# Optimization experiments

Measured on AMD Instinct MI355X. Metric: run time of the kernel, lower is better.

The kernel has to match this reference:

```python
import jax, jax.numpy as jnp
import numpy as np

B, S, D, H = 4, 2048, 1024, 16
HD = D // H

def _linear_params(key, fan_in, fan_out):
    kw, kb = jax.random.split(key)
    bound = 1.0 / np.sqrt(fan_in)
    W = jax.random.uniform(kw, (fan_in, fan_out), minval=-bound, maxval=bound, dtype=jnp.float32)
    b = jax.random.uniform(kb, (fan_out,), minval=-bound, maxval=bound, dtype=jnp.float32)
    return W, b

def setup_inputs() -> dict:
    key = jax.random.key(0)
    ks = jax.random.split(key, 7)
    query = jax.random.normal(ks[0], (B, S, D), dtype=jnp.float32)
    key_t = jax.random.normal(ks[1], (B, S, D), dtype=jnp.float32)
    value = jax.random.normal(ks[2], (B, S, D), dtype=jnp.float32)
    Wq, bq = _linear_params(ks[3], D, D)
    Wk, bk = _linear_params(ks[4], D, D)
    Wv, bv = _linear_params(ks[5], D, D)
    Wo, bo = _linear_params(ks[6], D, D)
    return {"query": query, "key": key_t, "value": value,
            "Wq": Wq, "bq": bq, "Wk": Wk, "bk": bk,
            "Wv": Wv, "bv": bv, "Wo": Wo, "bo": bo}

def reference(query, key, value, Wq, bq, Wk, bk, Wv, bv, Wo, bo):
    b, s, _ = query.shape
    scale = HD ** -0.5
    # project and split heads -> [b, h, s, hd]
    Q = (query @ Wq + bq).reshape(b, s, H, HD).transpose(0, 2, 1, 3)
    K = (key @ Wk + bk).reshape(b, s, H, HD).transpose(0, 2, 1, 3)
    V = (value @ Wv + bv).reshape(b, s, H, HD).transpose(0, 2, 1, 3)
    scores = jnp.einsum('bhqd,bhkd->bhqk', Q, K) * scale  # [b,h,s,s]
    attn = jax.nn.softmax(scores, axis=-1)
    out = jnp.einsum('bhqk,bhkd->bhqd', attn, V)
    out = out.transpose(0, 2, 1, 3).reshape(b, s, D)
    return out @ Wo + bo
```

## Files before the change

kernel.cpp:

```cpp
#include <hip/hip_runtime.h>

typedef unsigned short u16;
typedef __attribute__((ext_vector_type(8))) short short8;
typedef __attribute__((ext_vector_type(4))) float f32x4;
typedef __attribute__((ext_vector_type(4))) unsigned int u32x4;

union V8 { u32x4 u; short8 s; };

__device__ __forceinline__ u16 f2bf(float f) {
  union { float f; unsigned u; } v; v.f = f;
  unsigned r = v.u + 0x7fffu + ((v.u >> 16) & 1u);
  return (u16)(r >> 16);
}

__device__ __forceinline__ unsigned cvt_pk_bf16(float lo, float hi) {
  unsigned r;
  asm("v_cvt_pk_bf16_f32 %0, %1, %2" : "=v"(r) : "v"(lo), "v"(hi));
  return r;
}

__device__ __forceinline__ void gload_lds16(const void* g, void* l) {
  __builtin_amdgcn_global_load_lds((const __attribute__((address_space(1))) unsigned int*)g,
                                   (__attribute__((address_space(3))) unsigned int*)l, 16, 0, 0);
}

__device__ __forceinline__ f32x4 mfma16(short8 a, short8 b, f32x4 c) {
  return __builtin_amdgcn_mfma_f32_16x16x32_bf16(a, b, c, 0, 0, 0);
}

__global__ __launch_bounds__(256) void cvt3_kernel(const float* __restrict__ q,
                                                   const float* __restrict__ k,
                                                   const float* __restrict__ v,
                                                   u16* __restrict__ oq,
                                                   u16* __restrict__ ok,
                                                   u16* __restrict__ ov) {
  const int bid = blockIdx.x;
  const float* in = (bid < 4096) ? q : (bid < 8192 ? k : v);
  u16* out = (bid < 4096) ? oq : (bid < 8192 ? ok : ov);
  const size_t i = ((size_t)(bid & 4095) * 256 + threadIdx.x) * 8;
  const float4* p = (const float4*)(in + i);
  float4 a = p[0], b = p[1];
  u32x4 w;
  w[0] = cvt_pk_bf16(a.x, a.y); w[1] = cvt_pk_bf16(a.z, a.w);
  w[2] = cvt_pk_bf16(b.x, b.y); w[3] = cvt_pk_bf16(b.z, b.w);
  *(u32x4*)(out + i) = w;
}

__global__ __launch_bounds__(256) void wtrans4_kernel(const float* __restrict__ Wq, const float* __restrict__ Wk,
                                                      const float* __restrict__ Wv, const float* __restrict__ Wo,
                                                      u16* __restrict__ WtQ, u16* __restrict__ WtK,
                                                      u16* __restrict__ WtV, u16* __restrict__ WtO) {
  const int bid = blockIdx.x;
  const int wsel = bid >> 9;
  const float* W = (wsel == 0) ? Wq : (wsel == 1) ? Wk : (wsel == 2) ? Wv : Wo;
  u16* Wt = (wsel == 0) ? WtQ : (wsel == 1) ? WtK : (wsel == 2) ? WtV : WtO;
  const int tid = (bid & 511) * 256 + threadIdx.x;
  const int n = tid & 1023;
  const int kb = (tid >> 10) << 3;
  u32x4 w;
#pragma unroll
  for (int j = 0; j < 4; j++)
    w[j] = cvt_pk_bf16(W[(size_t)(kb + 2 * j) * 1024 + n], W[(size_t)(kb + 2 * j + 1) * 1024 + n]);
  *(u32x4*)(Wt + (size_t)n * 1024 + kb) = w;
}

__global__ __launch_bounds__(256) void gemm_qkv_kernel(const u16* __restrict__ A,
                                                       const u16* __restrict__ Wt,
                                                       const float* __restrict__ bq,
                                                       const float* __restrict__ bk,
                                                       const float* __restrict__ bv,
                                                       u16* __restrict__ Outs,
                                                       float qscale) {
  constexpr int K = 1024, N = 1024;
  __shared__ u16 Ash[2][4096];
  __shared__ u16 Bsh[2][4096];
  const int t = threadIdx.x;
  const int l = t & 63;
  const int w = t >> 6;
  const int wm = w >> 1, wn = w & 1;
  const int bid0 = blockIdx.x;
  const int swz = (bid0 & 7) * 192 + (bid0 >> 3);
  const int bm = swz >> 3, bn = swz & 7;
  const int m0 = bm * 128, n0 = bn * 128;
  const int sec = m0 >> 13;
  const u16* Bt = Wt + ((size_t)sec << 20);
  const float* bias = (sec == 0) ? bq : (sec == 1) ? bk : bv;
  const float outscale = (sec == 0) ? qscale : 1.0f;

  f32x4 acc[4][4];
#pragma unroll
  for (int i = 0; i < 4; i++)
#pragma unroll
    for (int j = 0; j < 4; j++) acc[i][j] = (f32x4){0.f, 0.f, 0.f, 0.f};

  const int line0 = t >> 3, c8 = t & 7;
  const int lc0 = c8 ^ (line0 & 7);
  const int row0 = 2 * line0 + (lc0 >> 2);
  const int kc0 = (lc0 & 3) << 3;
  const int line1 = line0 + 32;
  const int lc1 = c8 ^ (line1 & 7);
  const int row1 = 2 * line1 + (lc1 >> 2);
  const int kc1 = (lc1 & 3) << 3;

  const u16* Ab = A + (size_t)m0 * K;
  const u16* Bb = Bt + (size_t)n0 * K;

  int aoff[4], boff[4];
#pragma unroll
  for (int mt = 0; mt < 4; mt++) {
    int R = wm * 64 + mt * 16 + (l & 15);
    int cc = (((R & 1) << 2) + (l >> 4)) ^ ((R >> 1) & 7);
    aoff[mt] = (R >> 1) * 64 + cc * 8;
  }
#pragma unroll
  for (int nt = 0; nt < 4; nt++) {
    int R = wn * 64 + nt * 16 + (l & 15);
    int cc = (((R & 1) << 2) + (l >> 4)) ^ ((R >> 1) & 7);
    boff[nt] = (R >> 1) * 64 + cc * 8;
  }

  auto stage = [&](int buf, int k0) {
    u16* AW = &Ash[buf][w * 512];
    u16* BW = &Bsh[buf][w * 512];
    gload_lds16(Ab + (size_t)row0 * K + k0 + kc0, AW);
    gload_lds16(Ab + (size_t)row1 * K + k0 + kc1, AW + 2048);
    gload_lds16(Bb + (size_t)row0 * K + k0 + kc0, BW);
    gload_lds16(Bb + (size_t)row1 * K + k0 + kc1, BW + 2048);
  };

  stage(0, 0);
  __syncthreads();
  int cur = 0;
  for (int k0 = 0; k0 < K; k0 += 32) {
    if (k0 + 32 < K) stage(cur ^ 1, k0 + 32);
    short8 af[4], bfr[4];
#pragma unroll
    for (int mt = 0; mt < 4; mt++) af[mt] = *(const short8*)&Ash[cur][aoff[mt]];
#pragma unroll
    for (int nt = 0; nt < 4; nt++) bfr[nt] = *(const short8*)&Bsh[cur][boff[nt]];
#pragma unroll
    for (int mt = 0; mt < 4; mt++)
#pragma unroll
      for (int nt = 0; nt < 4; nt++)
        acc[mt][nt] = mfma16(af[mt], bfr[nt], acc[mt][nt]);
    __syncthreads();
    cur ^= 1;
  }

#pragma unroll
  for (int nt = 0; nt < 4; nt++) {
    const int n = n0 + wn * 64 + nt * 16 + (l & 15);
    const float bv2 = bias[n];
    if (sec < 2) {
      u16* C = Outs + ((size_t)sec << 23);
#pragma unroll
      for (int mt = 0; mt < 4; mt++) {
        const int m = (m0 & 8191) + wm * 64 + mt * 16 + ((l >> 4) << 2);
#pragma unroll
        for (int r = 0; r < 4; r++)
          C[(size_t)(m + r) * N + n] = f2bf((acc[mt][nt][r] + bv2) * outscale);
      }
    } else {
      const int mloc = m0 & 8191;
      const int b2 = mloc >> 11;
      const int h2 = n >> 6, d = n & 63;
      u16* C = Outs + ((size_t)2 << 23);
#pragma unroll
      for (int mt = 0; mt < 4; mt++) {
        const int s0 = (mloc & 2047) + wm * 64 + mt * 16 + ((l >> 4) << 2);
        const int u = s0 & 63;
        const int pos = ((((u >> 2) & 3) + ((u >> 5) & 1) * 4) << 3) + ((u >> 4) & 1) * 4;
        const int sp = (s0 & ~63) + pos;
        ushort4 pk;
        pk.x = f2bf(acc[mt][nt][0] + bv2);
        pk.y = f2bf(acc[mt][nt][1] + bv2);
        pk.z = f2bf(acc[mt][nt][2] + bv2);
        pk.w = f2bf(acc[mt][nt][3] + bv2);
        *(ushort4*)(C + (((size_t)((b2 * 16 + h2) * 64 + d)) << 11) + sp) = pk;
      }
    }
  }
}

__global__ __launch_bounds__(256) void gemm_out_kernel(const u16* __restrict__ A,
                                                       const u16* __restrict__ Bt,
                                                       const float* __restrict__ bias,
                                                       float* __restrict__ Cout) {
  constexpr int K = 1024, N = 1024;
  __shared__ u16 Ash[2][4096];
  __shared__ u16 Bsh[2][4096];
  const int t = threadIdx.x;
  const int l = t & 63;
  const int w = t >> 6;
  const int wm = w >> 1, wn = w & 1;
  const int bid0 = blockIdx.x;
  const int swz = (bid0 & 7) * 64 + (bid0 >> 3);
  const int bm = swz >> 3, bn = swz & 7;
  const int m0 = bm * 128, n0 = bn * 128;

  f32x4 acc[4][4];
#pragma unroll
  for (int i = 0; i < 4; i++)
#pragma unroll
    for (int j = 0; j < 4; j++) acc[i][j] = (f32x4){0.f, 0.f, 0.f, 0.f};

  const int line0 = t >> 3, c8 = t & 7;
  const int lc0 = c8 ^ (line0 & 7);
  const int row0 = 2 * line0 + (lc0 >> 2);
  const int kc0 = (lc0 & 3) << 3;
  const int line1 = line0 + 32;
  const int lc1 = c8 ^ (line1 & 7);
  const int row1 = 2 * line1 + (lc1 >> 2);
  const int kc1 = (lc1 & 3) << 3;

  const u16* Ab = A + (size_t)m0 * K;
  const u16* Bb = Bt + (size_t)n0 * K;

  int aoff[4], boff[4];
#pragma unroll
  for (int mt = 0; mt < 4; mt++) {
    int R = wm * 64 + mt * 16 + (l & 15);
    int cc = (((R & 1) << 2) + (l >> 4)) ^ ((R >> 1) & 7);
    aoff[mt] = (R >> 1) * 64 + cc * 8;
  }
#pragma unroll
  for (int nt = 0; nt < 4; nt++) {
    int R = wn * 64 + nt * 16 + (l & 15);
    int cc = (((R & 1) << 2) + (l >> 4)) ^ ((R >> 1) & 7);
    boff[nt] = (R >> 1) * 64 + cc * 8;
  }

  auto stage = [&](int buf, int k0) {
    u16* AW = &Ash[buf][w * 512];
    u16* BW = &Bsh[buf][w * 512];
    gload_lds16(Ab + (size_t)row0 * K + k0 + kc0, AW);
    gload_lds16(Ab + (size_t)row1 * K + k0 + kc1, AW + 2048);
    gload_lds16(Bb + (size_t)row0 * K + k0 + kc0, BW);
    gload_lds16(Bb + (size_t)row1 * K + k0 + kc1, BW + 2048);
  };

  stage(0, 0);
  __syncthreads();
  int cur = 0;
  for (int k0 = 0; k0 < K; k0 += 32) {
    if (k0 + 32 < K) stage(cur ^ 1, k0 + 32);
    short8 af[4], bfr[4];
#pragma unroll
    for (int mt = 0; mt < 4; mt++) af[mt] = *(const short8*)&Ash[cur][aoff[mt]];
#pragma unroll
    for (int nt = 0; nt < 4; nt++) bfr[nt] = *(const short8*)&Bsh[cur][boff[nt]];
#pragma unroll
    for (int mt = 0; mt < 4; mt++)
#pragma unroll
      for (int nt = 0; nt < 4; nt++)
        acc[mt][nt] = mfma16(af[mt], bfr[nt], acc[mt][nt]);
    __syncthreads();
    cur ^= 1;
  }

#pragma unroll
  for (int nt = 0; nt < 4; nt++) {
    const int n = n0 + wn * 64 + nt * 16 + (l & 15);
    const float bv2 = bias[n];
#pragma unroll
    for (int mt = 0; mt < 4; mt++) {
      const int m = m0 + wm * 64 + mt * 16 + ((l >> 4) << 2);
#pragma unroll
      for (int r = 0; r < 4; r++)
        Cout[(size_t)(m + r) * N + n] = acc[mt][nt][r] + bv2;
    }
  }
}

__device__ __forceinline__ void softmax_lite(const f32x4 (&s)[4], float& lsum,
                                             short8& pa0, short8& pa1) {
  float p[4][4];
#pragma unroll
  for (int c = 0; c < 4; c++)
#pragma unroll
    for (int r = 0; r < 4; r++) p[c][r] = __builtin_amdgcn_exp2f(s[c][r]);
  lsum += (((p[0][0] + p[0][1]) + (p[0][2] + p[0][3])) + ((p[1][0] + p[1][1]) + (p[1][2] + p[1][3])))
        + (((p[2][0] + p[2][1]) + (p[2][2] + p[2][3])) + ((p[3][0] + p[3][1]) + (p[3][2] + p[3][3])));
  V8 u0, u1;
  u0.u[0] = cvt_pk_bf16(p[0][0], p[0][1]); u0.u[1] = cvt_pk_bf16(p[0][2], p[0][3]);
  u0.u[2] = cvt_pk_bf16(p[1][0], p[1][1]); u0.u[3] = cvt_pk_bf16(p[1][2], p[1][3]);
  u1.u[0] = cvt_pk_bf16(p[2][0], p[2][1]); u1.u[1] = cvt_pk_bf16(p[2][2], p[2][3]);
  u1.u[2] = cvt_pk_bf16(p[3][0], p[3][1]); u1.u[3] = cvt_pk_bf16(p[3][2], p[3][3]);
  pa0 = u0.s; pa1 = u1.s;
}

__global__ __launch_bounds__(256) void attn_kernel(const u16* __restrict__ Qb,
                                                   const u16* __restrict__ Kb,
                                                   const u16* __restrict__ Vtb,
                                                   u16* __restrict__ AO) {
  __shared__ u16 Ksh[2][4096];
  __shared__ u16 Vsh[2][4096];
  const int t = threadIdx.x, l = t & 63, w = t >> 6;
  const int g = l >> 4, ql = l & 15;
  const int bid0 = blockIdx.x;
  const int bid = (bid0 & 7) * 128 + (bid0 >> 3);
  const int qt = bid & 15;
  const int bh = bid >> 4;
  const int h = bh & 15, b = bh >> 4;
  const int q0 = qt * 128 + w * 32;

  const u16* Qrow = Qb + ((size_t)b * 2048 + q0 + ql) * 1024 + h * 64 + g * 8;
  const short8 qA0 = *(const short8*)(Qrow);
  const short8 qA1 = *(const short8*)(Qrow + 32);
  const short8 qB0 = *(const short8*)(Qrow + 16 * 1024);
  const short8 qB1 = *(const short8*)(Qrow + 16 * 1024 + 32);

  float lA = 0.f, lB = 0.f;
  f32x4 oA[4], oB[4];
#pragma unroll
  for (int i = 0; i < 4; i++) { oA[i] = (f32x4){0.f, 0.f, 0.f, 0.f}; oB[i] = oA[i]; }

  const int srow0 = t >> 3, sc = t & 7;
  const int slc0 = sc ^ (srow0 & 7);
  const int srow1 = srow0 + 32, slc1 = sc ^ (srow1 & 7);
  const u16* Kbase = Kb + ((size_t)b * 2048) * 1024 + h * 64;
  const u16* Vbase = Vtb + ((size_t)(b * 16 + h) * 64) * 2048;

  auto stage = [&](int buf, int kk0) {
    u16* KW = &Ksh[buf][w * 512];
    u16* VW = &Vsh[buf][w * 512];
    gload_lds16(Kbase + (size_t)(kk0 + srow0) * 1024 + slc0 * 8, KW);
    gload_lds16(Kbase + (size_t)(kk0 + srow1) * 1024 + slc1 * 8, KW + 2048);
    gload_lds16(Vbase + (size_t)srow0 * 2048 + kk0 + slc0 * 8, VW);
    gload_lds16(Vbase + (size_t)srow1 * 2048 + kk0 + slc1 * 8, VW + 2048);
  };

  int voff0[4], voff1[4];
#pragma unroll
  for (int dt = 0; dt < 4; dt++) {
    const int d = dt * 16 + ql;
    voff0[dt] = d * 64 + ((g ^ (d & 7)) << 3);
    voff1[dt] = d * 64 + (((g + 4) ^ (d & 7)) << 3);
  }

  stage(0, 0);
  __syncthreads();
  int cur = 0;

  for (int kk0 = 0; kk0 < 2048; kk0 += 64) {
    if (kk0 + 64 < 2048) stage(cur ^ 1, kk0 + 64);
    const u16* KC = Ksh[cur];
    const u16* VC = Vsh[cur];

    f32x4 sA[4], sB[4];
    __builtin_amdgcn_s_setprio(1);
#pragma unroll
    for (int c = 0; c < 4; c++) {
      const int R = c * 16 + ql;
      const int x = R & 7;
      const short8 kf0 = *(const short8*)&KC[R * 64 + ((g ^ x) << 3)];
      const short8 kf1 = *(const short8*)&KC[R * 64 + (((g + 4) ^ x) << 3)];
      f32x4 z = (f32x4){0.f, 0.f, 0.f, 0.f};
      z = mfma16(kf0, qA0, z);
      sA[c] = mfma16(kf1, qA1, z);
      z = (f32x4){0.f, 0.f, 0.f, 0.f};
      z = mfma16(kf0, qB0, z);
      sB[c] = mfma16(kf1, qB1, z);
    }
    __builtin_amdgcn_s_setprio(0);

    short8 paA0, paA1, paB0, paB1;
    softmax_lite(sA, lA, paA0, paA1);
    softmax_lite(sB, lB, paB0, paB1);

    __builtin_amdgcn_s_setprio(1);
#pragma unroll
    for (int dt = 0; dt < 4; dt++) {
      const short8 vf0 = *(const short8*)&VC[voff0[dt]];
      const short8 vf1 = *(const short8*)&VC[voff1[dt]];
      oA[dt] = mfma16(paA0, vf0, oA[dt]);
      oA[dt] = mfma16(paA1, vf1, oA[dt]);
      oB[dt] = mfma16(paB0, vf0, oB[dt]);
      oB[dt] = mfma16(paB1, vf1, oB[dt]);
    }
    __builtin_amdgcn_s_setprio(0);
    __syncthreads();
    cur ^= 1;
  }

  lA += __shfl_xor(lA, 16); lA += __shfl_xor(lA, 32);
  lB += __shfl_xor(lB, 16); lB += __shfl_xor(lB, 32);
  const float iA = __builtin_amdgcn_rcpf(lA);
  const float iB = __builtin_amdgcn_rcpf(lB);
  const int sb = g << 2;
  const float iA0 = __shfl(iA, sb), iA1 = __shfl(iA, sb + 1);
  const float iA2 = __shfl(iA, sb + 2), iA3 = __shfl(iA, sb + 3);
  const float iB0 = __shfl(iB, sb), iB1 = __shfl(iB, sb + 1);
  const float iB2 = __shfl(iB, sb + 2), iB3 = __shfl(iB, sb + 3);
  u16* Arow = AO + ((size_t)b * 2048 + q0) * 1024 + h * 64;
#pragma unroll
  for (int dt = 0; dt < 4; dt++) {
    const int col = dt * 16 + ql;
    Arow[(size_t)(4 * g + 0) * 1024 + col] = f2bf(oA[dt][0] * iA0);
    Arow[(size_t)(4 * g + 1) * 1024 + col] = f2bf(oA[dt][1] * iA1);
    Arow[(size_t)(4 * g + 2) * 1024 + col] = f2bf(oA[dt][2] * iA2);
    Arow[(size_t)(4 * g + 3) * 1024 + col] = f2bf(oA[dt][3] * iA3);
    Arow[(size_t)(16 + 4 * g + 0) * 1024 + col] = f2bf(oB[dt][0] * iB0);
    Arow[(size_t)(16 + 4 * g + 1) * 1024 + col] = f2bf(oB[dt][1] * iB1);
    Arow[(size_t)(16 + 4 * g + 2) * 1024 + col] = f2bf(oB[dt][2] * iB2);
    Arow[(size_t)(16 + 4 * g + 3) * 1024 + col] = f2bf(oB[dt][3] * iB3);
  }
}

extern "C" void kernel_launch(void* const* d_in, const int* in_sizes, int n_in,
                              void* d_out, int out_size, void* d_ws, size_t ws_size,
                              hipStream_t stream) {
  (void)in_sizes; (void)n_in; (void)out_size; (void)ws_size;
  const float* query = (const float*)d_in[0];
  const float* key   = (const float*)d_in[1];
  const float* value = (const float*)d_in[2];
  const float* Wq = (const float*)d_in[3];  const float* bq = (const float*)d_in[4];
  const float* Wk = (const float*)d_in[5];  const float* bk = (const float*)d_in[6];
  const float* Wv = (const float*)d_in[7];  const float* bv = (const float*)d_in[8];
  const float* Wo = (const float*)d_in[9];  const float* bo = (const float*)d_in[10];
  float* out = (float*)d_out;

  const size_t SZX = (size_t)8192 * 1024;
  const size_t SZW = (size_t)1024 * 1024;
  u16* qin = (u16*)d_ws;
  u16* kin = qin + SZX;
  u16* vin = kin + SZX;
  u16* Qb  = vin + SZX;
  u16* Kbf = Qb + SZX;
  u16* Vtb = Kbf + SZX;
  u16* WtQ = Vtb + SZX;
  u16* WtK = WtQ + SZW;
  u16* WtV = WtK + SZW;
  u16* WtO = WtV + SZW;
  u16* AO  = qin;

  const float QSCALE = 0.125f * 1.44269504088896f;

  cvt3_kernel<<<12288, 256, 0, stream>>>(query, key, value, qin, kin, vin);
  wtrans4_kernel<<<2048, 256, 0, stream>>>(Wq, Wk, Wv, Wo, WtQ, WtK, WtV, WtO);

  gemm_qkv_kernel<<<1536, 256, 0, stream>>>(qin, WtQ, bq, bk, bv, Qb, QSCALE);

  attn_kernel<<<1024, 256, 0, stream>>>(Qb, Kbf, Vtb, AO);

  gemm_out_kernel<<<512, 256, 0, stream>>>(AO, WtO, bo, out);
}
```

Measured before the change: 337.8 us.

## Merge projection GEMMs into 256x128-tile kernel with triple-buffered interleaved staging

Replaces the two 128x128 GEMM kernels with one templated kernel that uses 256x128 tiles, a three-stage LDS ring buffer, and split staging interleaved between two MFMA half-steps with s_setprio and explicit vmcnt waits. Larger tiles raise operand reuse per LDS load, and the deeper pipeline aims to hide global-load latency. The cost is more accumulator registers and LDS per block. The output GEMM now launches only 256 blocks, which may underfill the 256 CUs.

```diff
diff --git a/kernel.cpp b/kernel.cpp
--- a/kernel.cpp
+++ b/kernel.cpp
@@ -64,210 +64,169 @@
   *(u32x4*)(Wt + (size_t)n * 1024 + kb) = w;
 }
 
-__global__ __launch_bounds__(256) void gemm_qkv_kernel(const u16* __restrict__ A,
-                                                       const u16* __restrict__ Wt,
-                                                       const float* __restrict__ bq,
-                                                       const float* __restrict__ bk,
-                                                       const float* __restrict__ bv,
-                                                       u16* __restrict__ Outs,
-                                                       float qscale) {
-  constexpr int K = 1024, N = 1024;
-  __shared__ u16 Ash[2][4096];
-  __shared__ u16 Bsh[2][4096];
-  const int t = threadIdx.x;
-  const int l = t & 63;
-  const int w = t >> 6;
+template <int IS_QKV>
+__global__ __launch_bounds__(256, 2) void gemm256_kernel(const u16* __restrict__ A,
+                                                         const u16* __restrict__ Wt,
+                                                         const float* __restrict__ bQ,
+                                                         const float* __restrict__ bK,
+                                                         const float* __restrict__ bV,
+                                                         void* __restrict__ Outs,
+                                                         float qscale) {
+  constexpr int K = 1024;
+  constexpr int NBM = IS_QKV ? 96 : 32;
+  constexpr int NT = 32;
+  __shared__ u16 Ash[3][8192];
+  __shared__ u16 Bsh[3][4096];
+  const int t = threadIdx.x, l = t & 63, w = t >> 6;
   const int wm = w >> 1, wn = w & 1;
-  const int bid0 = blockIdx.x;
-  const int swz = (bid0 & 7) * 192 + (bid0 >> 3);
-  const int bm = swz >> 3, bn = swz & 7;
-  const int m0 = bm * 128, n0 = bn * 128;
-  const int sec = m0 >> 13;
+  const int g = l >> 4, ql = l & 15;
+  const int bid = blockIdx.x;
+  const int s = (bid & 7) * NBM + (bid >> 3);
+  const int bm = s >> 3, bn = s & 7;
+  const int m0 = bm * 256, n0 = bn * 128;
+
+  const int sec = IS_QKV ? (bm >> 5) : 0;
   const u16* Bt = Wt + ((size_t)sec << 20);
-  const float* bias = (sec == 0) ? bq : (sec == 1) ? bk : bv;
-  const float outscale = (sec == 0) ? qscale : 1.0f;
-
-  f32x4 acc[4][4];
-#pragma unroll
-  for (int i = 0; i < 4; i++)
-#pragma unroll
-    for (int j = 0; j < 4; j++) acc[i][j] = (f32x4){0.f, 0.f, 0.f, 0.f};
-
-  const int line0 = t >> 3, c8 = t & 7;
-  const int lc0 = c8 ^ (line0 & 7);
-  const int row0 = 2 * line0 + (lc0 >> 2);
-  const int kc0 = (lc0 & 3) << 3;
-  const int line1 = line0 + 32;
-  const int lc1 = c8 ^ (line1 & 7);
-  const int row1 = 2 * line1 + (lc1 >> 2);
-  const int kc1 = (lc1 & 3) << 3;
-
   const u16* Ab = A + (size_t)m0 * K;
   const u16* Bb = Bt + (size_t)n0 * K;
 
-  int aoff[4], boff[4];
-#pragma unroll
-  for (int mt = 0; mt < 4; mt++) {
-    int R = wm * 64 + mt * 16 + (l & 15);
-    int cc = (((R & 1) << 2) + (l >> 4)) ^ ((R >> 1) & 7);
+  f32x4 acc[8][4];
+#pragma unroll
+  for (int i = 0; i < 8; i++)
+#pragma unroll
+    for (int j = 0; j < 4; j++) acc[i][j] = (f32x4){0.f, 0.f, 0.f, 0.f};
+
+  const int slc = (t & 7) ^ ((t >> 3) & 7);
+  const int srow = 2 * (t >> 3) + (slc >> 2);
+  const int skc = (slc & 3) << 3;
+
+  int aoff[8], boff[4];
+#pragma unroll
+  for (int mt = 0; mt < 8; mt++) {
+    const int R = wm * 128 + mt * 16 + ql;
+    const int cc = (((R & 1) << 2) + g) ^ ((R >> 1) & 7);
     aoff[mt] = (R >> 1) * 64 + cc * 8;
   }
 #pragma unroll
   for (int nt = 0; nt < 4; nt++) {
-    int R = wn * 64 + nt * 16 + (l & 15);
-    int cc = (((R & 1) << 2) + (l >> 4)) ^ ((R >> 1) & 7);
+    const int R = wn * 64 + nt * 16 + ql;
+    const int cc = (((R & 1) << 2) + g) ^ ((R >> 1) & 7);
     boff[nt] = (R >> 1) * 64 + cc * 8;
   }
 
-  auto stage = [&](int buf, int k0) {
-    u16* AW = &Ash[buf][w * 512];
-    u16* BW = &Bsh[buf][w * 512];
-    gload_lds16(Ab + (size_t)row0 * K + k0 + kc0, AW);
-    gload_lds16(Ab + (size_t)row1 * K + k0 + kc1, AW + 2048);
-    gload_lds16(Bb + (size_t)row0 * K + k0 + kc0, BW);
-    gload_lds16(Bb + (size_t)row1 * K + k0 + kc1, BW + 2048);
+  auto stA = [&](int buf, int k0s, int j) {
+    gload_lds16(Ab + (size_t)(srow + 64 * j) * K + k0s + skc, &Ash[buf][j * 2048 + w * 512]);
   };
-
-  stage(0, 0);
-  __syncthreads();
+  auto stB = [&](int buf, int k0s, int j) {
+    gload_lds16(Bb + (size_t)(srow + 64 * j) * K + k0s + skc, &Bsh[buf][j * 2048 + w * 512]);
+  };
+
+#pragma unroll
+  for (int j = 0; j < 4; j++) stA(0, 0, j);
+  stB(0, 0, 0); stB(0, 0, 1);
+#pragma unroll
+  for (int j = 0; j < 4; j++) stA(1, 32, j);
+  stB(1, 32, 0); stB(1, 32, 1);
+  asm volatile("s_waitcnt vmcnt(6)" ::: "memory");
+  __builtin_amdgcn_sched_barrier(0);
+  __builtin_amdgcn_s_barrier();
+
   int cur = 0;
-  for (int k0 = 0; k0 < K; k0 += 32) {
-    if (k0 + 32 < K) stage(cur ^ 1, k0 + 32);
-    short8 af[4], bfr[4];
-#pragma unroll
-    for (int mt = 0; mt < 4; mt++) af[mt] = *(const short8*)&Ash[cur][aoff[mt]];
-#pragma unroll
-    for (int nt = 0; nt < 4; nt++) bfr[nt] = *(const short8*)&Bsh[cur][boff[nt]];
-#pragma unroll
-    for (int mt = 0; mt < 4; mt++)
+  for (int T = 0; T < NT; ++T) {
+    const int stg = (cur >= 1) ? cur - 1 : cur + 2;
+    const bool doStage = (T + 2 < NT);
+    const int k0s = T * 32 + 64;
+    const u16* AC = Ash[cur];
+    const u16* BC = Bsh[cur];
+
+    short8 af[4], bf[4];
+#pragma unroll
+    for (int i = 0; i < 4; i++) af[i] = *(const short8*)&AC[aoff[i]];
+#pragma unroll
+    for (int i = 0; i < 4; i++) bf[i] = *(const short8*)&BC[boff[i]];
+    if (doStage) { stA(stg, k0s, 0); stA(stg, k0s, 1); stB(stg, k0s, 0); }
+    __builtin_amdgcn_s_barrier();
+    __builtin_amdgcn_s_setprio(1);
+#pragma unroll
+    for (int i = 0; i < 4; i++)
 #pragma unroll
       for (int nt = 0; nt < 4; nt++)
-        acc[mt][nt] = mfma16(af[mt], bfr[nt], acc[mt][nt]);
-    __syncthreads();
-    cur ^= 1;
-  }
-
-#pragma unroll
-  for (int nt = 0; nt < 4; nt++) {
-    const int n = n0 + wn * 64 + nt * 16 + (l & 15);
-    const float bv2 = bias[n];
-    if (sec < 2) {
-      u16* C = Outs + ((size_t)sec << 23);
-#pragma unroll
-      for (int mt = 0; mt < 4; mt++) {
-        const int m = (m0 & 8191) + wm * 64 + mt * 16 + ((l >> 4) << 2);
-#pragma unroll
-        for (int r = 0; r < 4; r++)
-          C[(size_t)(m + r) * N + n] = f2bf((acc[mt][nt][r] + bv2) * outscale);
-      }
-    } else {
-      const int mloc = m0 & 8191;
-      const int b2 = mloc >> 11;
-      const int h2 = n >> 6, d = n & 63;
-      u16* C = Outs + ((size_t)2 << 23);
-#pragma unroll
-      for (int mt = 0; mt < 4; mt++) {
-        const int s0 = (mloc & 2047) + wm * 64 + mt * 16 + ((l >> 4) << 2);
-        const int u = s0 & 63;
-        const int pos = ((((u >> 2) & 3) + ((u >> 5) & 1) * 4) << 3) + ((u >> 4) & 1) * 4;
-        const int sp = (s0 & ~63) + pos;
-        ushort4 pk;
-        pk.x = f2bf(acc[mt][nt][0] + bv2);
-        pk.y = f2bf(acc[mt][nt][1] + bv2);
-        pk.z = f2bf(acc[mt][nt][2] + bv2);
-        pk.w = f2bf(acc[mt][nt][3] + bv2);
-        *(ushort4*)(C + (((size_t)((b2 * 16 + h2) * 64 + d)) << 11) + sp) = pk;
+        acc[i][nt] = mfma16(af[i], bf[nt], acc[i][nt]);
+    __builtin_amdgcn_s_setprio(0);
+    __builtin_amdgcn_s_barrier();
+
+    short8 ag[4];
+#pragma unroll
+    for (int i = 0; i < 4; i++) ag[i] = *(const short8*)&AC[aoff[4 + i]];
+    if (doStage) { stA(stg, k0s, 2); stA(stg, k0s, 3); stB(stg, k0s, 1); }
+    __builtin_amdgcn_s_barrier();
+    __builtin_amdgcn_s_setprio(1);
+#pragma unroll
+    for (int i = 0; i < 4; i++)
+#pragma unroll
+      for (int nt = 0; nt < 4; nt++)
+        acc[4 + i][nt] = mfma16(ag[i], bf[nt], acc[4 + i][nt]);
+    __builtin_amdgcn_s_setprio(0);
+    if (T < NT - 2) {
+      asm volatile("s_waitcnt vmcnt(6)" ::: "memory");
+      __builtin_amdgcn_sched_barrier(0);
+    } else if (T == NT - 2) {
+      asm volatile("s_waitcnt vmcnt(0)" ::: "memory");
+      __builtin_amdgcn_sched_barrier(0);
+    }
+    __builtin_amdgcn_s_barrier();
+    cur = (cur == 2) ? 0 : cur + 1;
+  }
+
+  if constexpr (IS_QKV) {
+    const float* bias = (sec == 0) ? bQ : (sec == 1) ? bK : bV;
+    const float outscale = (sec == 0) ? qscale : 1.0f;
+    const int mloc = m0 & 8191;
+#pragma unroll
+    for (int nt = 0; nt < 4; nt++) {
+      const int n = n0 + wn * 64 + nt * 16 + ql;
+      const float bv2 = bias[n];
+      if (sec < 2) {
+        u16* C = (u16*)Outs + ((size_t)sec << 23);
+#pragma unroll
+        for (int mt = 0; mt < 8; mt++) {
+          const int m = mloc + wm * 128 + mt * 16 + (g << 2);
+#pragma unroll
+          for (int r = 0; r < 4; r++)
+            C[(size_t)(m + r) * 1024 + n] = f2bf((acc[mt][nt][r] + bv2) * outscale);
+        }
+      } else {
+        const int b2 = mloc >> 11;
+        const int h2 = n >> 6, d = n & 63;
+        u16* C = (u16*)Outs + ((size_t)2 << 23);
+#pragma unroll
+        for (int mt = 0; mt < 8; mt++) {
+          const int s0 = (mloc & 2047) + wm * 128 + mt * 16 + (g << 2);
+          const int u = s0 & 63;
+          const int pos = ((((u >> 2) & 3) + ((u >> 5) & 1) * 4) << 3) + ((u >> 4) & 1) * 4;
+          const int sp = (s0 & ~63) + pos;
+          ushort4 pk;
+          pk.x = f2bf(acc[mt][nt][0] + bv2);
+          pk.y = f2bf(acc[mt][nt][1] + bv2);
+          pk.z = f2bf(acc[mt][nt][2] + bv2);
+          pk.w = f2bf(acc[mt][nt][3] + bv2);
+          *(ushort4*)(C + (((size_t)((b2 * 16 + h2) * 64 + d)) << 11) + sp) = pk;
+        }
       }
     }
-  }
-}
-
-__global__ __launch_bounds__(256) void gemm_out_kernel(const u16* __restrict__ A,
-                                                       const u16* __restrict__ Bt,
-                                                       const float* __restrict__ bias,
-                                                       float* __restrict__ Cout) {
-  constexpr int K = 1024, N = 1024;
-  __shared__ u16 Ash[2][4096];
-  __shared__ u16 Bsh[2][4096];
-  const int t = threadIdx.x;
-  const int l = t & 63;
-  const int w = t >> 6;
-  const int wm = w >> 1, wn = w & 1;
-  const int bid0 = blockIdx.x;
-  const int swz = (bid0 & 7) * 64 + (bid0 >> 3);
-  const int bm = swz >> 3, bn = swz & 7;
-  const int m0 = bm * 128, n0 = bn * 128;
-
-  f32x4 acc[4][4];
-#pragma unroll
-  for (int i = 0; i < 4; i++)
-#pragma unroll
-    for (int j = 0; j < 4; j++) acc[i][j] = (f32x4){0.f, 0.f, 0.f, 0.f};
-
-  const int line0 = t >> 3, c8 = t & 7;
-  const int lc0 = c8 ^ (line0 & 7);
-  const int row0 = 2 * line0 + (lc0 >> 2);
-  const int kc0 = (lc0 & 3) << 3;
-  const int line1 = line0 + 32;
-  const int lc1 = c8 ^ (line1 & 7);
-  const int row1 = 2 * line1 + (lc1 >> 2);
-  const int kc1 = (lc1 & 3) << 3;
-
-  const u16* Ab = A + (size_t)m0 * K;
-  const u16* Bb = Bt + (size_t)n0 * K;
-
-  int aoff[4], boff[4];
-#pragma unroll
-  for (int mt = 0; mt < 4; mt++) {
-    int R = wm * 64 + mt * 16 + (l & 15);
-    int cc = (((R & 1) << 2) + (l >> 4)) ^ ((R >> 1) & 7);
-    aoff[mt] = (R >> 1) * 64 + cc * 8;
-  }
-#pragma unroll
-  for (int nt = 0; nt < 4; nt++) {
-    int R = wn * 64 + nt * 16 + (l & 15);
-    int cc = (((R & 1) << 2) + (l >> 4)) ^ ((R >> 1) & 7);
-    boff[nt] = (R >> 1) * 64 + cc * 8;
-  }
-
-  auto stage = [&](int buf, int k0) {
-    u16* AW = &Ash[buf][w * 512];
-    u16* BW = &Bsh[buf][w * 512];
-    gload_lds16(Ab + (size_t)row0 * K + k0 + kc0, AW);
-    gload_lds16(Ab + (size_t)row1 * K + k0 + kc1, AW + 2048);
-    gload_lds16(Bb + (size_t)row0 * K + k0 + kc0, BW);
-    gload_lds16(Bb + (size_t)row1 * K + k0 + kc1, BW + 2048);
-  };
-
-  stage(0, 0);
-  __syncthreads();
-  int cur = 0;
-  for (int k0 = 0; k0 < K; k0 += 32) {
-    if (k0 + 32 < K) stage(cur ^ 1, k0 + 32);
-    short8 af[4], bfr[4];
-#pragma unroll
-    for (int mt = 0; mt < 4; mt++) af[mt] = *(const short8*)&Ash[cur][aoff[mt]];
-#pragma unroll
-    for (int nt = 0; nt < 4; nt++) bfr[nt] = *(const short8*)&Bsh[cur][boff[nt]];
-#pragma unroll
-    for (int mt = 0; mt < 4; mt++)
-#pragma unroll
-      for (int nt = 0; nt < 4; nt++)
-        acc[mt][nt] = mfma16(af[mt], bfr[nt], acc[mt][nt]);
-    __syncthreads();
-    cur ^= 1;
-  }
-
-#pragma unroll
-  for (int nt = 0; nt < 4; nt++) {
-    const int n = n0 + wn * 64 + nt * 16 + (l & 15);
-    const float bv2 = bias[n];
-#pragma unroll
-    for (int mt = 0; mt < 4; mt++) {
-      const int m = m0 + wm * 64 + mt * 16 + ((l >> 4) << 2);
-#pragma unroll
-      for (int r = 0; r < 4; r++)
-        Cout[(size_t)(m + r) * N + n] = acc[mt][nt][r] + bv2;
+  } else {
+    float* C = (float*)Outs;
+#pragma unroll
+    for (int nt = 0; nt < 4; nt++) {
+      const int n = n0 + wn * 64 + nt * 16 + ql;
+      const float bv2 = bQ[n];
+#pragma unroll
+      for (int mt = 0; mt < 8; mt++) {
+        const int m = m0 + wm * 128 + mt * 16 + (g << 2);
+#pragma unroll
+        for (int r = 0; r < 4; r++)
+          C[(size_t)(m + r) * 1024 + n] = acc[mt][nt][r] + bv2;
+      }
     }
   }
 }
@@ -439,9 +398,9 @@
   cvt3_kernel<<<12288, 256, 0, stream>>>(query, key, value, qin, kin, vin);
   wtrans4_kernel<<<2048, 256, 0, stream>>>(Wq, Wk, Wv, Wo, WtQ, WtK, WtV, WtO);
 
-  gemm_qkv_kernel<<<1536, 256, 0, stream>>>(qin, WtQ, bq, bk, bv, Qb, QSCALE);
+  gemm256_kernel<1><<<768, 256, 0, stream>>>(qin, WtQ, bq, bk, bv, (void*)Qb, QSCALE);
 
   attn_kernel<<<1024, 256, 0, stream>>>(Qb, Kbf, Vtb, AO);
 
-  gemm_out_kernel<<<512, 256, 0, stream>>>(AO, WtO, bo, out);
-}
+  gemm256_kernel<0><<<256, 256, 0, stream>>>(AO, WtO, bo, bo, bo, (void*)out, 1.0f);
+}
```

Result: slower. 344.9 us (+2.1%).
